# Kernel optimization log

Hardware: AMD Instinct MI355X
Metric: run time of the kernel (lower is better)

Reference implementation:

```python
import jax, jax.numpy as jnp
import numpy as np

B, LS, LH, D1, D2 = 16, 1024, 1024, 1024, 1024


def setup_inputs() -> dict:
    key = jax.random.key(0)
    k1, k2, k3 = jax.random.split(key, 3)
    S = jax.random.normal(k1, (B, LS, D1), dtype=jnp.float32)
    H = jax.random.normal(k2, (B, LH, D2), dtype=jnp.float32)
    pad_mask = jnp.zeros((B, LS, LH), dtype=jnp.float32)  # additive mask
    W_w = jax.random.normal(k3, (D2, D1), dtype=jnp.float32) / np.sqrt(D1)
    W_b = jnp.zeros((D2,), dtype=jnp.float32)
    return {"S": S, "H": H, "pad_mask": pad_mask, "W_w": W_w, "W_b": W_b}


def reference(S, H, pad_mask, W_w, W_b):
    # Linear projection: S_ = S @ W^T + b  -> [B, LS, D2]
    S_ = jnp.einsum('bsd,ed->bse', S, W_w) + W_b
    # Unscaled dot-product scores: [B, LS, LH]
    score = jnp.einsum('bse,bte->bst', S_, H)
    score = score + pad_mask  # additive pad mask
    score = jax.nn.softmax(score, axis=-1)
    # Weighted sum of H: [B, LS, D2]
    out = jnp.einsum('bst,bte->bse', score, H)
    return out
```

## Files before the change

kernel.cpp:

```cpp
#include <hip/hip_runtime.h>
#include <stdint.h>

typedef _Float16 half8 __attribute__((ext_vector_type(8)));
typedef float floatx4 __attribute__((ext_vector_type(4)));

__device__ __forceinline__ uint16_t f16bits(_Float16 h) {
  union { _Float16 f; uint16_t u; } x; x.f = h; return x.u;
}

__device__ __forceinline__ void g2l16(const void* g, void* l) {
  __builtin_amdgcn_global_load_lds((const __attribute__((address_space(1))) void*)g,
                                   (__attribute__((address_space(3))) void*)l,
                                   16, 0, 0);
}

__global__ __launch_bounds__(256) void split_f16_kernel(
    const float* __restrict__ x, uint16_t* __restrict__ hi,
    uint16_t* __restrict__ lo, int n4) {
  int i = blockIdx.x * 256 + threadIdx.x;
  if (i >= n4) return;
  float4 v = ((const float4*)x)[i];
  ushort4 h, l;
  _Float16 a;
  a = (_Float16)v.x; h.x = f16bits(a); l.x = f16bits((_Float16)(v.x - (float)a));
  a = (_Float16)v.y; h.y = f16bits(a); l.y = f16bits((_Float16)(v.y - (float)a));
  a = (_Float16)v.z; h.z = f16bits(a); l.z = f16bits((_Float16)(v.z - (float)a));
  a = (_Float16)v.w; h.w = f16bits(a); l.w = f16bits((_Float16)(v.w - (float)a));
  ((ushort4*)hi)[i] = h;
  ((ushort4*)lo)[i] = l;
}

template <bool SPLIT, int MODE>
__global__ __launch_bounds__(256) void gemm_bt(
    const uint16_t* __restrict__ Ahi, const uint16_t* __restrict__ Alo,
    const uint16_t* __restrict__ Bhi, const uint16_t* __restrict__ Blo,
    uint16_t* __restrict__ Chi, uint16_t* __restrict__ Clo,
    float* __restrict__ Cf, const float* __restrict__ mask,
    const float* __restrict__ bias, int N, int K,
    long batchA, long batchB, long batchC) {
  constexpr int NBUF = SPLIT ? 2 : 1;
  constexpr int LOI = SPLIT ? 1 : 0;
  __shared__ __align__(16) uint16_t sA[NBUF][128 * 32];
  __shared__ __align__(16) uint16_t sB[NBUF][128 * 32];

  const int tid = threadIdx.x;
  const int lane = tid & 63;
  const int w = tid >> 6;
  const int wr = w >> 1, wc = w & 1;
  const int quad = lane >> 4, l16 = lane & 15;

  const int m0 = blockIdx.y * 128;
  const int n0 = blockIdx.x * 128;
  const size_t zA = (size_t)blockIdx.z * batchA;
  const size_t zB = (size_t)blockIdx.z * batchB;
  const size_t zC = (size_t)blockIdx.z * batchC;

  const int r0 = w * 32 + (lane >> 2);
  const int ldc = (lane & 3) * 16;

  const char* gAh0 = (const char*)(Ahi + zA + (size_t)(m0 + r0) * K) + ldc;
  const char* gAh1 = gAh0 + (size_t)16 * K * 2;
  const char* gBh0 = (const char*)(Bhi + zB + (size_t)(n0 + r0) * K) + ldc;
  const char* gBh1 = gBh0 + (size_t)16 * K * 2;
  const char* gAl0 = gAh0; const char* gAl1 = gAh1;
  const char* gBl0 = gBh0; const char* gBl1 = gBh1;
  if constexpr (SPLIT) {
    gAl0 = (const char*)(Alo + zA + (size_t)(m0 + r0) * K) + ldc;
    gAl1 = gAl0 + (size_t)16 * K * 2;
    gBl0 = (const char*)(Blo + zB + (size_t)(n0 + r0) * K) + ldc;
    gBl1 = gBl0 + (size_t)16 * K * 2;
  }
  uint16_t* lA0 = &sA[0][(w * 32) * 32];
  uint16_t* lA1 = &sA[0][(w * 32 + 16) * 32];
  uint16_t* lB0 = &sB[0][(w * 32) * 32];
  uint16_t* lB1 = &sB[0][(w * 32 + 16) * 32];
  uint16_t* lA0l = &sA[LOI][(w * 32) * 32];
  uint16_t* lA1l = &sA[LOI][(w * 32 + 16) * 32];
  uint16_t* lB0l = &sB[LOI][(w * 32) * 32];
  uint16_t* lB1l = &sB[LOI][(w * 32 + 16) * 32];

  const int aoff = (wr * 64 + l16) * 32 + quad * 8;
  const int boff = (wc * 64 + l16) * 32 + quad * 8;

  floatx4 acc[4][4];
  floatx4 zero = {0.f, 0.f, 0.f, 0.f};
#pragma unroll
  for (int i = 0; i < 4; ++i)
#pragma unroll
    for (int j = 0; j < 4; ++j) acc[i][j] = zero;

  const int nkt = K >> 5;
  for (int kt = 0; kt < nkt; ++kt) {
    const int kb = kt * 64;
    g2l16(gAh0 + kb, lA0);
    g2l16(gAh1 + kb, lA1);
    g2l16(gBh0 + kb, lB0);
    g2l16(gBh1 + kb, lB1);
    if constexpr (SPLIT) {
      g2l16(gAl0 + kb, lA0l);
      g2l16(gAl1 + kb, lA1l);
      g2l16(gBl0 + kb, lB0l);
      g2l16(gBl1 + kb, lB1l);
    }
    __syncthreads();

    half8 ah[4], bh[4], al[4], bl[4];
#pragma unroll
    for (int i = 0; i < 4; ++i) {
      ah[i] = *(const half8*)&sA[0][aoff + i * 512];
      bh[i] = *(const half8*)&sB[0][boff + i * 512];
      if constexpr (SPLIT) {
        al[i] = *(const half8*)&sA[1][aoff + i * 512];
        bl[i] = *(const half8*)&sB[1][boff + i * 512];
      }
    }
#pragma unroll
    for (int i = 0; i < 4; ++i)
#pragma unroll
      for (int j = 0; j < 4; ++j) {
        if constexpr (SPLIT) {
          acc[i][j] = __builtin_amdgcn_mfma_f32_16x16x32_f16(al[i], bh[j], acc[i][j], 0, 0, 0);
          acc[i][j] = __builtin_amdgcn_mfma_f32_16x16x32_f16(ah[i], bl[j], acc[i][j], 0, 0, 0);
        }
        acc[i][j] = __builtin_amdgcn_mfma_f32_16x16x32_f16(ah[i], bh[j], acc[i][j], 0, 0, 0);
      }
    __syncthreads();
  }

  const int crow0 = m0 + wr * 64 + quad * 4;
  const int ccol0 = n0 + wc * 64 + l16;
#pragma unroll
  for (int j = 0; j < 4; ++j) {
    const int col = ccol0 + j * 16;
    float bj = 0.f;
    if constexpr (MODE == 0) bj = bias[col];
#pragma unroll
    for (int i = 0; i < 4; ++i) {
#pragma unroll
      for (int r = 0; r < 4; ++r) {
        const int row = crow0 + i * 16 + r;
        const size_t idx = zC + (size_t)row * N + col;
        float v = acc[i][j][r];
        if constexpr (MODE == 0) {
          v += bj;
          _Float16 h = (_Float16)v;
          Chi[idx] = f16bits(h);
          Clo[idx] = f16bits((_Float16)(v - (float)h));
        } else if constexpr (MODE == 1) {
          Cf[idx] = v + mask[idx];
        } else {
          Cf[idx] = v;
        }
      }
    }
  }
}

__global__ __launch_bounds__(256) void softmax_kernel(
    const float* __restrict__ sc, uint16_t* __restrict__ p) {
  const int row = blockIdx.x;
  const float* x = sc + (size_t)row * 1024;
  const int t = threadIdx.x;
  float4 v = ((const float4*)x)[t];
  float m = fmaxf(fmaxf(v.x, v.y), fmaxf(v.z, v.w));
#pragma unroll
  for (int off = 32; off; off >>= 1) m = fmaxf(m, __shfl_xor(m, off));
  __shared__ float redm[4];
  __shared__ float reds[4];
  const int wv = t >> 6, ln = t & 63;
  if (ln == 0) redm[wv] = m;
  __syncthreads();
  m = fmaxf(fmaxf(redm[0], redm[1]), fmaxf(redm[2], redm[3]));
  float e0 = __expf(v.x - m), e1 = __expf(v.y - m);
  float e2 = __expf(v.z - m), e3 = __expf(v.w - m);
  float s = e0 + e1 + e2 + e3;
#pragma unroll
  for (int off = 32; off; off >>= 1) s += __shfl_xor(s, off);
  if (ln == 0) reds[wv] = s;
  __syncthreads();
  s = reds[0] + reds[1] + reds[2] + reds[3];
  float inv = 1.f / s;
  ushort4 o;
  o.x = f16bits((_Float16)(e0 * inv));
  o.y = f16bits((_Float16)(e1 * inv));
  o.z = f16bits((_Float16)(e2 * inv));
  o.w = f16bits((_Float16)(e3 * inv));
  ((ushort4*)(p + (size_t)row * 1024))[t] = o;
}

__global__ __launch_bounds__(256) void transpose_f16_kernel(
    const float* __restrict__ src, uint16_t* __restrict__ dst) {
  __shared__ uint16_t tile[64][65];
  const int e0 = blockIdx.x * 64;
  const int t0 = blockIdx.y * 64;
  const size_t bb = (size_t)blockIdx.z << 20;
  const int r = threadIdx.x >> 4;
  const int c = (threadIdx.x & 15) * 4;
#pragma unroll
  for (int it = 0; it < 4; ++it) {
    const int tr = r + it * 16;
    float4 v = *(const float4*)(src + bb + (size_t)(t0 + tr) * 1024 + e0 + c);
    tile[c + 0][tr] = f16bits((_Float16)v.x);
    tile[c + 1][tr] = f16bits((_Float16)v.y);
    tile[c + 2][tr] = f16bits((_Float16)v.z);
    tile[c + 3][tr] = f16bits((_Float16)v.w);
  }
  __syncthreads();
#pragma unroll
  for (int it = 0; it < 4; ++it) {
    const int er = r + it * 16;
    ushort4 o;
    o.x = tile[er][c + 0];
    o.y = tile[er][c + 1];
    o.z = tile[er][c + 2];
    o.w = tile[er][c + 3];
    *(ushort4*)(dst + bb + (size_t)(e0 + er) * 1024 + t0 + c) = o;
  }
}

extern "C" void kernel_launch(void* const* d_in, const int* in_sizes, int n_in,
                              void* d_out, int out_size, void* d_ws, size_t ws_size,
                              hipStream_t stream) {
  (void)in_sizes; (void)n_in; (void)out_size; (void)ws_size;
  const float* S    = (const float*)d_in[0];
  const float* H    = (const float*)d_in[1];
  const float* mask = (const float*)d_in[2];
  const float* Ww   = (const float*)d_in[3];
  const float* Wb   = (const float*)d_in[4];
  float* out = (float*)d_out;
  char* ws = (char*)d_ws;
  const size_t MB = 1024ull * 1024ull;

  uint16_t* Whi  = (uint16_t*)(ws + 0 * MB);
  uint16_t* Wlo  = (uint16_t*)(ws + 2 * MB);
  uint16_t* Pjhi = (uint16_t*)(ws + 4 * MB);
  uint16_t* Pjlo = (uint16_t*)(ws + 36 * MB);
  uint16_t* Hhi  = (uint16_t*)(ws + 68 * MB);
  uint16_t* Hlo  = (uint16_t*)(ws + 100 * MB);
  uint16_t* Shi  = (uint16_t*)(ws + 132 * MB);
  uint16_t* Slo  = (uint16_t*)(ws + 164 * MB);
  float*    SC   = (float*)(ws + 132 * MB);
  uint16_t* PR   = (uint16_t*)(ws + 68 * MB);
  uint16_t* HT   = (uint16_t*)(ws + 100 * MB);

  split_f16_kernel<<<16384, 256, 0, stream>>>(S, Shi, Slo, 4 * 1024 * 1024);
  split_f16_kernel<<<16384, 256, 0, stream>>>(H, Hhi, Hlo, 4 * 1024 * 1024);
  split_f16_kernel<<<1024, 256, 0, stream>>>(Ww, Whi, Wlo, 256 * 1024);

  gemm_bt<true, 0><<<dim3(8, 128, 1), 256, 0, stream>>>(
      Shi, Slo, Whi, Wlo, Pjhi, Pjlo, nullptr, nullptr, Wb,
      1024, 1024, 0, 0, 0);
  gemm_bt<true, 1><<<dim3(8, 8, 16), 256, 0, stream>>>(
      Pjhi, Pjlo, Hhi, Hlo, nullptr, nullptr, SC, mask, nullptr,
      1024, 1024, 1048576, 1048576, 1048576);
  softmax_kernel<<<16384, 256, 0, stream>>>(SC, PR);
  transpose_f16_kernel<<<dim3(16, 16, 16), 256, 0, stream>>>(H, HT);
  gemm_bt<false, 2><<<dim3(8, 8, 16), 256, 0, stream>>>(
      PR, nullptr, HT, nullptr, nullptr, nullptr, out, nullptr, nullptr,
      1024, 1024, 1048576, 1048576, 1048576);
}
```

Measured before the change: 600.6 us.

## XOR-swizzle LDS tiles, stage split-f16 MFMA passes, request higher occupancy

The global-to-LDS copies and the fragment reads now use a matching XOR swizzle on the 16-byte column chunk, to cut LDS bank conflicts on the fragment reads. The split-precision inner loop is reordered into three passes (A_hi*B_lo, A_hi*B_hi, A_lo*B_hi) so that only a few fragment arrays are live at any time, which lowers register pressure. The launch bounds now ask for 4 blocks per CU. The risk is that the occupancy hint forces register spills, and the swizzle must match the fragment layout exactly.

```diff
diff --git a/kernel.cpp b/kernel.cpp
--- a/kernel.cpp
+++ b/kernel.cpp
@@ -31,7 +31,7 @@
 }
 
 template <bool SPLIT, int MODE>
-__global__ __launch_bounds__(256) void gemm_bt(
+__global__ __launch_bounds__(256, 4) void gemm_bt(
     const uint16_t* __restrict__ Ahi, const uint16_t* __restrict__ Alo,
     const uint16_t* __restrict__ Bhi, const uint16_t* __restrict__ Blo,
     uint16_t* __restrict__ Chi, uint16_t* __restrict__ Clo,
@@ -56,7 +56,7 @@
   const size_t zC = (size_t)blockIdx.z * batchC;
 
   const int r0 = w * 32 + (lane >> 2);
-  const int ldc = (lane & 3) * 16;
+  const int ldc = (((lane & 3) ^ ((lane >> 2) & 3)) * 16);
 
   const char* gAh0 = (const char*)(Ahi + zA + (size_t)(m0 + r0) * K) + ldc;
   const char* gAh1 = gAh0 + (size_t)16 * K * 2;
@@ -79,8 +79,8 @@
   uint16_t* lB0l = &sB[LOI][(w * 32) * 32];
   uint16_t* lB1l = &sB[LOI][(w * 32 + 16) * 32];
 
-  const int aoff = (wr * 64 + l16) * 32 + quad * 8;
-  const int boff = (wc * 64 + l16) * 32 + quad * 8;
+  const int aoff = (wr * 64 + l16) * 32 + ((quad ^ (l16 & 3)) * 8);
+  const int boff = (wc * 64 + l16) * 32 + ((quad ^ (l16 & 3)) * 8);
 
   floatx4 acc[4][4];
   floatx4 zero = {0.f, 0.f, 0.f, 0.f};
@@ -104,26 +104,37 @@
     }
     __syncthreads();
 
-    half8 ah[4], bh[4], al[4], bl[4];
-#pragma unroll
-    for (int i = 0; i < 4; ++i) {
-      ah[i] = *(const half8*)&sA[0][aoff + i * 512];
-      bh[i] = *(const half8*)&sB[0][boff + i * 512];
-      if constexpr (SPLIT) {
-        al[i] = *(const half8*)&sA[1][aoff + i * 512];
-        bl[i] = *(const half8*)&sB[1][boff + i * 512];
-      }
-    }
+    half8 fa[4];
+#pragma unroll
+    for (int i = 0; i < 4; ++i) fa[i] = *(const half8*)&sA[0][aoff + i * 512];
+    if constexpr (SPLIT) {
+      half8 fbl[4];
+#pragma unroll
+      for (int j = 0; j < 4; ++j) fbl[j] = *(const half8*)&sB[1][boff + j * 512];
+#pragma unroll
+      for (int i = 0; i < 4; ++i)
+#pragma unroll
+        for (int j = 0; j < 4; ++j)
+          acc[i][j] = __builtin_amdgcn_mfma_f32_16x16x32_f16(fa[i], fbl[j], acc[i][j], 0, 0, 0);
+    }
+    half8 fbh[4];
+#pragma unroll
+    for (int j = 0; j < 4; ++j) fbh[j] = *(const half8*)&sB[0][boff + j * 512];
 #pragma unroll
     for (int i = 0; i < 4; ++i)
 #pragma unroll
-      for (int j = 0; j < 4; ++j) {
-        if constexpr (SPLIT) {
-          acc[i][j] = __builtin_amdgcn_mfma_f32_16x16x32_f16(al[i], bh[j], acc[i][j], 0, 0, 0);
-          acc[i][j] = __builtin_amdgcn_mfma_f32_16x16x32_f16(ah[i], bl[j], acc[i][j], 0, 0, 0);
-        }
-        acc[i][j] = __builtin_amdgcn_mfma_f32_16x16x32_f16(ah[i], bh[j], acc[i][j], 0, 0, 0);
-      }
+      for (int j = 0; j < 4; ++j)
+        acc[i][j] = __builtin_amdgcn_mfma_f32_16x16x32_f16(fa[i], fbh[j], acc[i][j], 0, 0, 0);
+    if constexpr (SPLIT) {
+      half8 fal[4];
+#pragma unroll
+      for (int i = 0; i < 4; ++i) fal[i] = *(const half8*)&sA[1][aoff + i * 512];
+#pragma unroll
+      for (int i = 0; i < 4; ++i)
+#pragma unroll
+        for (int j = 0; j < 4; ++j)
+          acc[i][j] = __builtin_amdgcn_mfma_f32_16x16x32_f16(fal[i], fbh[j], acc[i][j], 0, 0, 0);
+    }
     __syncthreads();
   }
 
```

Result: faster. 582.2 us (-3.1%).
